# Kernel tuning notes

Hardware: AMD Instinct MI355X
Metric: run time of the kernel (lower is better)

## Reference

```python
import jax, jax.numpy as jnp
import numpy as np
from jax import lax

B, S, T = 32, 128, 128
E, H = 256, 512
VS, VT = 16000, 16000


def _gru_cell(h, x, Wih, Whh, bih, bhh):
    # PyTorch GRU gate order: r, z, n
    gi = x @ Wih.T + bih            # [B, 3H]
    gh = h @ Whh.T + bhh            # [B, 3H]
    ir, iz, inn = jnp.split(gi, 3, axis=-1)
    hr, hz, hn = jnp.split(gh, 3, axis=-1)
    r = jax.nn.sigmoid(ir + hr)
    z = jax.nn.sigmoid(iz + hz)
    n = jnp.tanh(inn + r * hn)
    return (1.0 - z) * n + z * h


def setup_inputs() -> dict:
    key = jax.random.key(0)
    ks = jax.random.split(key, 16)
    s = 0.05
    emb_src = (jax.random.normal(ks[2], (VS, E)) * s).at[0].set(0.0)  # padding_idx=0
    emb_tgt = (jax.random.normal(ks[3], (VT, E)) * s).at[0].set(0.0)
    return {
        "src": jax.random.randint(ks[0], (B, S), 0, VS),
        "tgt": jax.random.randint(ks[1], (B, T), 0, VT),
        "emb_src": emb_src,
        "emb_tgt": emb_tgt,
        "enc_Wih": jax.random.normal(ks[4], (3 * H, E)) * s,
        "enc_Whh": jax.random.normal(ks[5], (3 * H, H)) * s,
        "enc_bih": jnp.zeros((3 * H,), jnp.float32),
        "enc_bhh": jnp.zeros((3 * H,), jnp.float32),
        "dec_Wih": jax.random.normal(ks[6], (3 * H, E + H)) * s,
        "dec_Whh": jax.random.normal(ks[7], (3 * H, H)) * s,
        "dec_bih": jnp.zeros((3 * H,), jnp.float32),
        "dec_bhh": jnp.zeros((3 * H,), jnp.float32),
        "attn_W": jax.random.normal(ks[8], (H, 2 * H)) * s,   # nn.Linear(2H, H)
        "attn_b": jnp.zeros((H,), jnp.float32),
        "attn_v": jax.random.normal(ks[9], (H,)) * s,          # nn.Linear(H, 1, bias=False)
        "fc_W": jax.random.normal(ks[10], (VT, H)) * s,
        "fc_b": jnp.zeros((VT,), jnp.float32),
    }


def reference(src, tgt, emb_src, emb_tgt,
              enc_Wih, enc_Whh, enc_bih, enc_bhh,
              dec_Wih, dec_Whh, dec_bih, dec_bhh,
              attn_W, attn_b, attn_v, fc_W, fc_b):
    xs = emb_src[src]              # [B, S, E]
    ys = emb_tgt[tgt]              # [B, T, E]
    bsz = src.shape[0]

    # ---- encoder: single-layer GRU over src ----
    h0 = jnp.zeros((bsz, H), xs.dtype)

    def enc_step(h, x_t):
        h2 = _gru_cell(h, x_t, enc_Wih, enc_Whh, enc_bih, enc_bhh)
        return h2, h2

    h_enc, enc_seq = lax.scan(enc_step, h0, xs.transpose(1, 0, 2))
    enc_out = enc_seq.transpose(1, 0, 2)  # [B, S, H]

    # split attn weight: cat((hidden, enc_out)) @ W.T = h @ Wh.T + enc @ We.T
    Wh, We = attn_W[:, :H], attn_W[:, H:]
    enc_proj = enc_out @ We.T + attn_b    # [B, S, H], precomputed once

    # ---- decoder: per-step attention + GRU cell ----
    def dec_step(h, y_t):
        energy = jnp.tanh((h @ Wh.T)[:, None, :] + enc_proj)   # [B, S, H]
        scores = energy @ attn_v                               # [B, S]
        w = jax.nn.softmax(scores, axis=1)
        ctx = jnp.einsum('bs,bsh->bh', w, enc_out)             # [B, H]
        x = jnp.concatenate([y_t, ctx], axis=-1)               # [B, E+H]
        h2 = _gru_cell(h, x, dec_Wih, dec_Whh, dec_bih, dec_bhh)
        return h2, h2

    _, dec_seq = lax.scan(dec_step, h_enc, ys.transpose(1, 0, 2))
    dec_out = dec_seq.transpose(1, 0, 2)  # [B, T, H]

    logits = dec_out @ fc_W.T + fc_b      # [B, T, VT]
    return logits
```

## Files before the change

### kernel.cpp

```cpp
#include <hip/hip_runtime.h>
#include <hip/hip_bf16.h>

using bf16 = __hip_bfloat16;
typedef short bf16x8_t __attribute__((ext_vector_type(8)));
typedef float f32x4_t __attribute__((ext_vector_type(4)));

#define Bsz 32
#define Ssz 128
#define Tsz 128
#define Esz 256
#define Hsz 512
#define VTsz 16000

__device__ inline float sigm(float x)      { return 1.f / (1.f + __expf(-x)); }
__device__ inline float tanh_fast(float x) { return 1.f - 2.f / (1.f + __expf(2.f * x)); }

__device__ inline unsigned pack2(float x, float y) {
  unsigned short lo = __builtin_bit_cast(unsigned short, __float2bfloat16(x));
  unsigned short hi = __builtin_bit_cast(unsigned short, __float2bfloat16(y));
  return (unsigned)lo | ((unsigned)hi << 16);
}

__device__ inline uint4 f32x8_to_bf16x8(const float* s) {
  float4 a = *(const float4*)s;
  float4 b = *(const float4*)(s + 4);
  uint4 r;
  r.x = pack2(a.x, a.y); r.y = pack2(a.z, a.w);
  r.z = pack2(b.x, b.y); r.w = pack2(b.z, b.w);
  return r;
}

__global__ __launch_bounds__(256) void embed_gather(
    const int* __restrict__ src, const int* __restrict__ tgt,
    const float* __restrict__ es, const float* __restrict__ et,
    bf16* __restrict__ xs_b, bf16* __restrict__ ys_b)
{
  int idx = blockIdx.x * 256 + threadIdx.x;
  int which = idx >> 17;
  int c = idx & 131071;
  int row = c >> 5;
  int cc = c & 31;
  if (which == 0) {
    int tok = src[row];
    *(uint4*)(xs_b + (size_t)row * Esz + cc * 8) =
        f32x8_to_bf16x8(es + (size_t)tok * Esz + cc * 8);
  } else {
    int tok = tgt[row];
    *(uint4*)(ys_b + (size_t)row * Esz + cc * 8) =
        f32x8_to_bf16x8(et + (size_t)tok * Esz + cc * 8);
  }
}

__global__ __launch_bounds__(256) void transpose_w(
    const float* __restrict__ enc_Whh, const float* __restrict__ dec_Whh,
    const float* __restrict__ attn_W,  const float* __restrict__ dec_Wih,
    bf16* __restrict__ encWhh_t, bf16* __restrict__ Wcat_t, bf16* __restrict__ Wihctx_t)
{
  int idx = blockIdx.x * 256 + threadIdx.x;
  const int N1 = 512 * 1536, N2 = 512 * 2048;
  if (idx < N1) {
    int k = idx / 1536, j = idx % 1536;
    encWhh_t[idx] = __float2bfloat16(enc_Whh[(size_t)j * 512 + k]);
  } else if (idx < N1 + N2) {
    int r = idx - N1;
    int k = r / 2048, j = r % 2048;
    float v = (j < 1536) ? dec_Whh[(size_t)j * 512 + k]
                         : attn_W[(size_t)(j - 1536) * 1024 + k];
    Wcat_t[r] = __float2bfloat16(v);
  } else {
    int r = idx - N1 - N2;
    int k = r / 1536, j = r % 1536;
    Wihctx_t[r] = __float2bfloat16(dec_Wih[(size_t)j * 768 + 256 + k]);
  }
}

__global__ __launch_bounds__(256) void pack_weights(
    const float* __restrict__ enc_Wih, const float* __restrict__ dec_Wih,
    const float* __restrict__ attn_W,  const float* __restrict__ fc_W,
    bf16* __restrict__ encWih_b, bf16* __restrict__ decWihY_b,
    bf16* __restrict__ attnWe_b, bf16* __restrict__ fcW_b)
{
  int idx = blockIdx.x * 256 + threadIdx.x;
  const int R1 = 1536 * 256, R2 = 1536 * 256, R3 = 512 * 512;
  if (idx < R1) {
    encWih_b[idx] = __float2bfloat16(enc_Wih[idx]);
  } else if (idx < R1 + R2) {
    int r = idx - R1;
    int row = r >> 8, col = r & 255;
    decWihY_b[r] = __float2bfloat16(dec_Wih[(size_t)row * 768 + col]);
  } else if (idx < R1 + R2 + R3) {
    int r = idx - R1 - R2;
    int row = r >> 9, col = r & 511;
    attnWe_b[r] = __float2bfloat16(attn_W[(size_t)row * 1024 + 512 + col]);
  } else {
    int r = idx - R1 - R2 - R3;
    fcW_b[r] = __float2bfloat16(fc_W[r]);
  }
}

__global__ __launch_bounds__(256) void gemm_bt(
    const bf16* __restrict__ A, int lda,
    const bf16* __restrict__ B, int ldb,
    float* __restrict__ C, int ldc,
    const float* __restrict__ bias, int K)
{
  __shared__ __align__(16) bf16 As[128 * 64];
  __shared__ __align__(16) bf16 Bs[128 * 64];
  const int tid = threadIdx.x;
  const int m0 = blockIdx.y * 128, n0 = blockIdx.x * 128;
  const int lane = tid & 63, wave = tid >> 6;
  const int wm = (wave >> 1) * 64, wn = (wave & 1) * 64;
  const int fr = lane & 15, quad = lane >> 4;

  f32x4_t acc[4][4];
  const f32x4_t zero = {0.f, 0.f, 0.f, 0.f};
#pragma unroll
  for (int i = 0; i < 4; ++i)
#pragma unroll
    for (int j = 0; j < 4; ++j) acc[i][j] = zero;

  for (int k0 = 0; k0 < K; k0 += 64) {
    __syncthreads();
#pragma unroll
    for (int j = 0; j < 4; ++j) {
      int c = j * 256 + tid;
      int row = c >> 3, cc = c & 7;
      *(uint4*)(As + row * 64 + cc * 8) =
          *(const uint4*)(A + (size_t)(m0 + row) * lda + k0 + cc * 8);
      *(uint4*)(Bs + row * 64 + cc * 8) =
          *(const uint4*)(B + (size_t)(n0 + row) * ldb + k0 + cc * 8);
    }
    __syncthreads();
#pragma unroll
    for (int kk = 0; kk < 64; kk += 32) {
      bf16x8_t af[4], bfr[4];
#pragma unroll
      for (int mt = 0; mt < 4; ++mt)
        af[mt] = *(const bf16x8_t*)(As + (wm + mt * 16 + fr) * 64 + kk + quad * 8);
#pragma unroll
      for (int nt = 0; nt < 4; ++nt)
        bfr[nt] = *(const bf16x8_t*)(Bs + (wn + nt * 16 + fr) * 64 + kk + quad * 8);
#pragma unroll
      for (int mt = 0; mt < 4; ++mt)
#pragma unroll
        for (int nt = 0; nt < 4; ++nt)
          acc[mt][nt] = __builtin_amdgcn_mfma_f32_16x16x32_bf16(
              af[mt], bfr[nt], acc[mt][nt], 0, 0, 0);
    }
  }

#pragma unroll
  for (int mt = 0; mt < 4; ++mt) {
#pragma unroll
    for (int nt = 0; nt < 4; ++nt) {
      int n = n0 + wn + nt * 16 + fr;
      float bv = bias[n];
#pragma unroll
      for (int r = 0; r < 4; ++r) {
        int m = m0 + wm + mt * 16 + quad * 4 + r;
        C[(size_t)m * ldc + n] = acc[mt][nt][r] + bv;
      }
    }
  }
}

__global__ __launch_bounds__(256) void enc_step(
    const float* __restrict__ enc_gi, const bf16* __restrict__ Wt,
    const float* __restrict__ bhh, float* __restrict__ enc_out,
    bf16* __restrict__ enc_out_b, int t)
{
  __shared__ float hs[Hsz];
  __shared__ float ps[4][3][64];
  const int b = blockIdx.x >> 3, it = blockIdx.x & 7;
  const int tid = threadIdx.x, il = tid & 63, kg = tid >> 6;

  if (t == 0) {
    for (int i = tid; i < Hsz; i += 256) hs[i] = 0.f;
  } else {
    const float* hsrc = enc_out + ((size_t)b * Ssz + (t - 1)) * Hsz;
    for (int i = tid; i < Hsz; i += 256) hs[i] = hsrc[i];
  }
  __syncthreads();

  const int i = it * 64 + il;
  float pr = 0.f, pz = 0.f, pn = 0.f;
  for (int k = kg * 128; k < kg * 128 + 128; ++k) {
    const float hv = hs[k];
    const bf16* w = Wt + (size_t)k * 1536;
    pr += hv * (float)w[i];
    pz += hv * (float)w[Hsz + i];
    pn += hv * (float)w[2 * Hsz + i];
  }
  ps[kg][0][il] = pr; ps[kg][1][il] = pz; ps[kg][2][il] = pn;
  __syncthreads();

  if (tid < 64) {
    float ghr = ps[0][0][il] + ps[1][0][il] + ps[2][0][il] + ps[3][0][il] + bhh[i];
    float ghz = ps[0][1][il] + ps[1][1][il] + ps[2][1][il] + ps[3][1][il] + bhh[Hsz + i];
    float ghn = ps[0][2][il] + ps[1][2][il] + ps[2][2][il] + ps[3][2][il] + bhh[2 * Hsz + i];
    const float* gi = enc_gi + ((size_t)b * Ssz + t) * 1536;
    const float r = sigm(gi[i] + ghr);
    const float z = sigm(gi[Hsz + i] + ghz);
    const float n = tanh_fast(gi[2 * Hsz + i] + r * ghn);
    const float h2 = (1.f - z) * n + z * hs[i];
    const size_t o = ((size_t)b * Ssz + t) * Hsz + i;
    enc_out[o] = h2;
    enc_out_b[o] = __float2bfloat16(h2);
  }
}

__global__ __launch_bounds__(256) void dec_k1(
    const float* __restrict__ enc_out, const float* __restrict__ dec_seq,
    const bf16* __restrict__ Wcat_t, const float* __restrict__ dbhh,
    float* __restrict__ gh_ws, float* __restrict__ hW_ws, int t)
{
  __shared__ float hs[Hsz];
  __shared__ float ps[4][64];
  const int b = blockIdx.x >> 5, jt = blockIdx.x & 31;
  const int tid = threadIdx.x, il = tid & 63, kg = tid >> 6;

  const float* hsrc = (t == 0) ? (enc_out + ((size_t)b * Ssz + (Ssz - 1)) * Hsz)
                               : (dec_seq + ((size_t)b * Tsz + (t - 1)) * Hsz);
  for (int i = tid; i < Hsz; i += 256) hs[i] = hsrc[i];
  __syncthreads();

  const int j = jt * 64 + il;
  float p = 0.f;
  for (int k = kg * 128; k < kg * 128 + 128; ++k)
    p += hs[k] * (float)Wcat_t[(size_t)k * 2048 + j];
  ps[kg][il] = p;
  __syncthreads();

  if (tid < 64) {
    float s = ps[0][il] + ps[1][il] + ps[2][il] + ps[3][il];
    if (j < 1536) gh_ws[b * 1536 + j] = s + dbhh[j];
    else          hW_ws[b * Hsz + (j - 1536)] = s;
  }
}

__global__ __launch_bounds__(512) void dec_k2(
    const float* __restrict__ hW_ws, const float* __restrict__ enc_proj,
    const float* __restrict__ enc_out, const float* __restrict__ attn_v,
    float* __restrict__ ctx_ws)
{
  __shared__ float hw[Hsz], vv[Hsz], sc[Ssz], red[2], red2[2];
  const int b = blockIdx.x, tid = threadIdx.x;
  for (int i = tid; i < Hsz; i += 512) { hw[i] = hW_ws[b * Hsz + i]; vv[i] = attn_v[i]; }
  __syncthreads();

  const int wv = tid >> 6, lane = tid & 63;
  for (int s = wv; s < Ssz; s += 8) {
    const float* ep = enc_proj + ((size_t)b * Ssz + s) * Hsz;
    float pp = 0.f;
#pragma unroll
    for (int q = 0; q < 8; ++q) {
      int i = q * 64 + lane;
      pp += tanh_fast(hw[i] + ep[i]) * vv[i];
    }
#pragma unroll
    for (int off = 32; off; off >>= 1) pp += __shfl_down(pp, off);
    if (lane == 0) sc[s] = pp;
  }
  __syncthreads();

  if (tid < 128) {
    float v = sc[tid];
#pragma unroll
    for (int off = 32; off; off >>= 1) v = fmaxf(v, __shfl_down(v, off));
    if (lane == 0) red[tid >> 6] = v;
  }
  __syncthreads();
  const float mx = fmaxf(red[0], red[1]);
  if (tid < 128) {
    float e = __expf(sc[tid] - mx);
    sc[tid] = e;
    float v = e;
#pragma unroll
    for (int off = 32; off; off >>= 1) v += __shfl_down(v, off);
    if (lane == 0) red2[tid >> 6] = v;
  }
  __syncthreads();
  const float inv = 1.f / (red2[0] + red2[1]);

  for (int i = tid; i < Hsz; i += 512) {
    float a = 0.f;
    for (int s = 0; s < Ssz; ++s) a += sc[s] * enc_out[((size_t)b * Ssz + s) * Hsz + i];
    ctx_ws[b * Hsz + i] = a * inv;
  }
}

__global__ __launch_bounds__(256) void dec_k3(
    const float* __restrict__ ctx_ws, const bf16* __restrict__ Wihctx_t,
    const float* __restrict__ dec_gi_y, const float* __restrict__ gh_ws,
    const float* __restrict__ enc_out, float* __restrict__ dec_seq,
    bf16* __restrict__ dec_out_b, int t)
{
  __shared__ float cs[Hsz];
  __shared__ float ps[4][3][64];
  const int b = blockIdx.x >> 3, it = blockIdx.x & 7;
  const int tid = threadIdx.x, il = tid & 63, kg = tid >> 6;

  for (int i = tid; i < Hsz; i += 256) cs[i] = ctx_ws[b * Hsz + i];
  __syncthreads();

  const int i = it * 64 + il;
  float pr = 0.f, pz = 0.f, pn = 0.f;
  for (int k = kg * 128; k < kg * 128 + 128; ++k) {
    const float c = cs[k];
    const bf16* w = Wihctx_t + (size_t)k * 1536;
    pr += c * (float)w[i];
    pz += c * (float)w[Hsz + i];
    pn += c * (float)w[2 * Hsz + i];
  }
  ps[kg][0][il] = pr; ps[kg][1][il] = pz; ps[kg][2][il] = pn;
  __syncthreads();

  if (tid < 64) {
    const float* giy = dec_gi_y + ((size_t)b * Tsz + t) * 1536;
    const float* gh  = gh_ws + b * 1536;
    float gir = giy[i]           + ps[0][0][il] + ps[1][0][il] + ps[2][0][il] + ps[3][0][il];
    float giz = giy[Hsz + i]     + ps[0][1][il] + ps[1][1][il] + ps[2][1][il] + ps[3][1][il];
    float gin = giy[2 * Hsz + i] + ps[0][2][il] + ps[1][2][il] + ps[2][2][il] + ps[3][2][il];
    float ghr = gh[i], ghz = gh[Hsz + i], ghn = gh[2 * Hsz + i];
    const float* hsrc = (t == 0) ? (enc_out + ((size_t)b * Ssz + (Ssz - 1)) * Hsz)
                                 : (dec_seq + ((size_t)b * Tsz + (t - 1)) * Hsz);
    float hp = hsrc[i];
    const float r = sigm(gir + ghr);
    const float z = sigm(giz + ghz);
    const float n = tanh_fast(gin + r * ghn);
    const float h2 = (1.f - z) * n + z * hp;
    const size_t o = ((size_t)b * Tsz + t) * Hsz + i;
    dec_seq[o] = h2;
    dec_out_b[o] = __float2bfloat16(h2);
  }
}

extern "C" void kernel_launch(void* const* d_in, const int* in_sizes, int n_in,
                              void* d_out, int out_size, void* d_ws, size_t ws_size,
                              hipStream_t stream) {
  const int*   src      = (const int*)d_in[0];
  const int*   tgt      = (const int*)d_in[1];
  const float* emb_src  = (const float*)d_in[2];
  const float* emb_tgt  = (const float*)d_in[3];
  const float* enc_Wih  = (const float*)d_in[4];
  const float* enc_Whh  = (const float*)d_in[5];
  const float* enc_bih  = (const float*)d_in[6];
  const float* enc_bhh  = (const float*)d_in[7];
  const float* dec_Wih  = (const float*)d_in[8];
  const float* dec_Whh  = (const float*)d_in[9];
  const float* dec_bih  = (const float*)d_in[10];
  const float* dec_bhh  = (const float*)d_in[11];
  const float* attn_W   = (const float*)d_in[12];
  const float* attn_b   = (const float*)d_in[13];
  const float* attn_v   = (const float*)d_in[14];
  const float* fc_W     = (const float*)d_in[15];
  const float* fc_b     = (const float*)d_in[16];
  float* out = (float*)d_out;

  char* p = (char*)d_ws;
  auto alloc = [&](size_t n) { char* r = p; p += (n + 255) & ~(size_t)255; return r; };
  float* enc_gi    = (float*)alloc(4096ull * 1536 * 4);
  float* dec_gi_y  = (float*)alloc(4096ull * 1536 * 4);
  float* enc_out   = (float*)alloc(4096ull * 512 * 4);
  float* enc_proj  = (float*)alloc(4096ull * 512 * 4);
  float* dec_seq   = (float*)alloc(4096ull * 512 * 4);
  bf16*  enc_out_b = (bf16*)alloc(4096ull * 512 * 2);
  bf16*  dec_out_b = (bf16*)alloc(4096ull * 512 * 2);
  bf16*  xs_b      = (bf16*)alloc(4096ull * 256 * 2);
  bf16*  ys_b      = (bf16*)alloc(4096ull * 256 * 2);
  bf16*  encWhh_t  = (bf16*)alloc(512ull * 1536 * 2);
  bf16*  Wcat_t    = (bf16*)alloc(512ull * 2048 * 2);
  bf16*  Wihctx_t  = (bf16*)alloc(512ull * 1536 * 2);
  bf16*  encWih_b  = (bf16*)alloc(1536ull * 256 * 2);
  bf16*  decWihY_b = (bf16*)alloc(1536ull * 256 * 2);
  bf16*  attnWe_b  = (bf16*)alloc(512ull * 512 * 2);
  bf16*  fcW_b     = (bf16*)alloc(16000ull * 512 * 2);
  float* gh_ws     = (float*)alloc(32ull * 1536 * 4);
  float* hW_ws     = (float*)alloc(32ull * 512 * 4);
  float* ctx_ws    = (float*)alloc(32ull * 512 * 4);

  embed_gather<<<1024, 256, 0, stream>>>(src, tgt, emb_src, emb_tgt, xs_b, ys_b);
  transpose_w<<<10240, 256, 0, stream>>>(enc_Whh, dec_Whh, attn_W, dec_Wih,
                                         encWhh_t, Wcat_t, Wihctx_t);
  pack_weights<<<36096, 256, 0, stream>>>(enc_Wih, dec_Wih, attn_W, fc_W,
                                          encWih_b, decWihY_b, attnWe_b, fcW_b);

  gemm_bt<<<dim3(12, 32), 256, 0, stream>>>(xs_b, 256, encWih_b, 256,
                                            enc_gi, 1536, enc_bih, 256);
  gemm_bt<<<dim3(12, 32), 256, 0, stream>>>(ys_b, 256, decWihY_b, 256,
                                            dec_gi_y, 1536, dec_bih, 256);

  for (int t = 0; t < Ssz; ++t)
    enc_step<<<256, 256, 0, stream>>>(enc_gi, encWhh_t, enc_bhh, enc_out, enc_out_b, t);

  gemm_bt<<<dim3(4, 32), 256, 0, stream>>>(enc_out_b, 512, attnWe_b, 512,
                                           enc_proj, 512, attn_b, 512);

  for (int t = 0; t < Tsz; ++t) {
    dec_k1<<<1024, 256, 0, stream>>>(enc_out, dec_seq, Wcat_t, dec_bhh, gh_ws, hW_ws, t);
    dec_k2<<<32, 512, 0, stream>>>(hW_ws, enc_proj, enc_out, attn_v, ctx_ws);
    dec_k3<<<256, 256, 0, stream>>>(ctx_ws, Wihctx_t, dec_gi_y, gh_ws, enc_out,
                                    dec_seq, dec_out_b, t);
  }

  gemm_bt<<<dim3(125, 32), 256, 0, stream>>>(dec_out_b, 512, fcW_b, 512,
                                             out, VTsz, fc_b, 512);
}
```

Baseline: 5.728 ms.

## Replace per-timestep kernel launches with persistent cooperative kernels using grid sync

Folds the 128 encoder-step launches and the 384 decoder-step launches into two persistent cooperative kernels of 256 blocks each, with grid.sync() between dependent phases. This removes per-launch overhead and the inter-kernel gaps in the recurrent loops. The decoder's first phase now uses 256 blocks, each thread doing a full 512-length dot product instead of a 4-way split-K over 1024 blocks, so that phase has less parallelism. The attention phase runs on only 32 blocks while the rest wait at the grid barrier.

```diff
diff --git a/kernel.cpp b/kernel.cpp
--- a/kernel.cpp
+++ b/kernel.cpp
@@ -1,5 +1,8 @@
 #include <hip/hip_runtime.h>
 #include <hip/hip_bf16.h>
+#include <hip/hip_cooperative_groups.h>
+
+namespace cg = cooperative_groups;
 
 using bf16 = __hip_bfloat16;
 typedef short bf16x8_t __attribute__((ext_vector_type(8)));
@@ -164,174 +167,175 @@
   }
 }
 
-__global__ __launch_bounds__(256) void enc_step(
+__global__ __launch_bounds__(256) void enc_loop(
     const float* __restrict__ enc_gi, const bf16* __restrict__ Wt,
     const float* __restrict__ bhh, float* __restrict__ enc_out,
-    bf16* __restrict__ enc_out_b, int t)
-{
+    bf16* __restrict__ enc_out_b)
+{
+  cg::grid_group grid = cg::this_grid();
   __shared__ float hs[Hsz];
   __shared__ float ps[4][3][64];
   const int b = blockIdx.x >> 3, it = blockIdx.x & 7;
   const int tid = threadIdx.x, il = tid & 63, kg = tid >> 6;
-
-  if (t == 0) {
-    for (int i = tid; i < Hsz; i += 256) hs[i] = 0.f;
-  } else {
-    const float* hsrc = enc_out + ((size_t)b * Ssz + (t - 1)) * Hsz;
-    for (int i = tid; i < Hsz; i += 256) hs[i] = hsrc[i];
-  }
+  const int i = it * 64 + il;
+
+  for (int k = tid; k < Hsz; k += 256) hs[k] = 0.f;
   __syncthreads();
 
-  const int i = it * 64 + il;
-  float pr = 0.f, pz = 0.f, pn = 0.f;
-  for (int k = kg * 128; k < kg * 128 + 128; ++k) {
-    const float hv = hs[k];
-    const bf16* w = Wt + (size_t)k * 1536;
-    pr += hv * (float)w[i];
-    pz += hv * (float)w[Hsz + i];
-    pn += hv * (float)w[2 * Hsz + i];
-  }
-  ps[kg][0][il] = pr; ps[kg][1][il] = pz; ps[kg][2][il] = pn;
-  __syncthreads();
-
-  if (tid < 64) {
-    float ghr = ps[0][0][il] + ps[1][0][il] + ps[2][0][il] + ps[3][0][il] + bhh[i];
-    float ghz = ps[0][1][il] + ps[1][1][il] + ps[2][1][il] + ps[3][1][il] + bhh[Hsz + i];
-    float ghn = ps[0][2][il] + ps[1][2][il] + ps[2][2][il] + ps[3][2][il] + bhh[2 * Hsz + i];
-    const float* gi = enc_gi + ((size_t)b * Ssz + t) * 1536;
-    const float r = sigm(gi[i] + ghr);
-    const float z = sigm(gi[Hsz + i] + ghz);
-    const float n = tanh_fast(gi[2 * Hsz + i] + r * ghn);
-    const float h2 = (1.f - z) * n + z * hs[i];
-    const size_t o = ((size_t)b * Ssz + t) * Hsz + i;
-    enc_out[o] = h2;
-    enc_out_b[o] = __float2bfloat16(h2);
-  }
-}
-
-__global__ __launch_bounds__(256) void dec_k1(
-    const float* __restrict__ enc_out, const float* __restrict__ dec_seq,
-    const bf16* __restrict__ Wcat_t, const float* __restrict__ dbhh,
-    float* __restrict__ gh_ws, float* __restrict__ hW_ws, int t)
-{
+  for (int t = 0; t < Ssz; ++t) {
+    float pr = 0.f, pz = 0.f, pn = 0.f;
+    for (int k = kg * 128; k < kg * 128 + 128; ++k) {
+      const float hv = hs[k];
+      const bf16* w = Wt + (size_t)k * 1536;
+      pr += hv * (float)w[i];
+      pz += hv * (float)w[Hsz + i];
+      pn += hv * (float)w[2 * Hsz + i];
+    }
+    ps[kg][0][il] = pr; ps[kg][1][il] = pz; ps[kg][2][il] = pn;
+    __syncthreads();
+
+    if (tid < 64) {
+      float ghr = ps[0][0][il] + ps[1][0][il] + ps[2][0][il] + ps[3][0][il] + bhh[i];
+      float ghz = ps[0][1][il] + ps[1][1][il] + ps[2][1][il] + ps[3][1][il] + bhh[Hsz + i];
+      float ghn = ps[0][2][il] + ps[1][2][il] + ps[2][2][il] + ps[3][2][il] + bhh[2 * Hsz + i];
+      const float* gi = enc_gi + ((size_t)b * Ssz + t) * 1536;
+      const float r = sigm(gi[i] + ghr);
+      const float z = sigm(gi[Hsz + i] + ghz);
+      const float n = tanh_fast(gi[2 * Hsz + i] + r * ghn);
+      const float h2 = (1.f - z) * n + z * hs[i];
+      const size_t o = ((size_t)b * Ssz + t) * Hsz + i;
+      enc_out[o] = h2;
+      enc_out_b[o] = __float2bfloat16(h2);
+    }
+    grid.sync();
+
+    if (t + 1 < Ssz) {
+      const float* hsrc = enc_out + ((size_t)b * Ssz + t) * Hsz;
+      for (int k = tid; k < Hsz; k += 256) hs[k] = hsrc[k];
+      __syncthreads();
+    }
+  }
+}
+
+__global__ __launch_bounds__(256) void dec_loop(
+    const float* __restrict__ enc_out, const float* __restrict__ enc_proj,
+    const bf16* __restrict__ Wcat_t, const bf16* __restrict__ Wihctx_t,
+    const float* __restrict__ dec_gi_y, const float* __restrict__ dbhh,
+    const float* __restrict__ attn_v, float* __restrict__ dec_seq,
+    bf16* __restrict__ dec_out_b, float* __restrict__ gh_ws,
+    float* __restrict__ hW_ws, float* __restrict__ ctx_ws)
+{
+  cg::grid_group grid = cg::this_grid();
+  const int bid = blockIdx.x, tid = threadIdx.x;
+
+  const int b1 = bid >> 3, jt = bid & 7, j = jt * 256 + tid;
+  const int il = tid & 63, kg = tid >> 6;
+  const int i3 = (bid & 7) * 64 + il;
+
   __shared__ float hs[Hsz];
-  __shared__ float ps[4][64];
-  const int b = blockIdx.x >> 5, jt = blockIdx.x & 31;
-  const int tid = threadIdx.x, il = tid & 63, kg = tid >> 6;
-
-  const float* hsrc = (t == 0) ? (enc_out + ((size_t)b * Ssz + (Ssz - 1)) * Hsz)
-                               : (dec_seq + ((size_t)b * Tsz + (t - 1)) * Hsz);
-  for (int i = tid; i < Hsz; i += 256) hs[i] = hsrc[i];
-  __syncthreads();
-
-  const int j = jt * 64 + il;
-  float p = 0.f;
-  for (int k = kg * 128; k < kg * 128 + 128; ++k)
-    p += hs[k] * (float)Wcat_t[(size_t)k * 2048 + j];
-  ps[kg][il] = p;
-  __syncthreads();
-
-  if (tid < 64) {
-    float s = ps[0][il] + ps[1][il] + ps[2][il] + ps[3][il];
-    if (j < 1536) gh_ws[b * 1536 + j] = s + dbhh[j];
-    else          hW_ws[b * Hsz + (j - 1536)] = s;
-  }
-}
-
-__global__ __launch_bounds__(512) void dec_k2(
-    const float* __restrict__ hW_ws, const float* __restrict__ enc_proj,
-    const float* __restrict__ enc_out, const float* __restrict__ attn_v,
-    float* __restrict__ ctx_ws)
-{
-  __shared__ float hw[Hsz], vv[Hsz], sc[Ssz], red[2], red2[2];
-  const int b = blockIdx.x, tid = threadIdx.x;
-  for (int i = tid; i < Hsz; i += 512) { hw[i] = hW_ws[b * Hsz + i]; vv[i] = attn_v[i]; }
-  __syncthreads();
-
-  const int wv = tid >> 6, lane = tid & 63;
-  for (int s = wv; s < Ssz; s += 8) {
-    const float* ep = enc_proj + ((size_t)b * Ssz + s) * Hsz;
-    float pp = 0.f;
-#pragma unroll
-    for (int q = 0; q < 8; ++q) {
-      int i = q * 64 + lane;
-      pp += tanh_fast(hw[i] + ep[i]) * vv[i];
-    }
-#pragma unroll
-    for (int off = 32; off; off >>= 1) pp += __shfl_down(pp, off);
-    if (lane == 0) sc[s] = pp;
-  }
-  __syncthreads();
-
-  if (tid < 128) {
-    float v = sc[tid];
-#pragma unroll
-    for (int off = 32; off; off >>= 1) v = fmaxf(v, __shfl_down(v, off));
-    if (lane == 0) red[tid >> 6] = v;
-  }
-  __syncthreads();
-  const float mx = fmaxf(red[0], red[1]);
-  if (tid < 128) {
-    float e = __expf(sc[tid] - mx);
-    sc[tid] = e;
-    float v = e;
-#pragma unroll
-    for (int off = 32; off; off >>= 1) v += __shfl_down(v, off);
-    if (lane == 0) red2[tid >> 6] = v;
-  }
-  __syncthreads();
-  const float inv = 1.f / (red2[0] + red2[1]);
-
-  for (int i = tid; i < Hsz; i += 512) {
-    float a = 0.f;
-    for (int s = 0; s < Ssz; ++s) a += sc[s] * enc_out[((size_t)b * Ssz + s) * Hsz + i];
-    ctx_ws[b * Hsz + i] = a * inv;
-  }
-}
-
-__global__ __launch_bounds__(256) void dec_k3(
-    const float* __restrict__ ctx_ws, const bf16* __restrict__ Wihctx_t,
-    const float* __restrict__ dec_gi_y, const float* __restrict__ gh_ws,
-    const float* __restrict__ enc_out, float* __restrict__ dec_seq,
-    bf16* __restrict__ dec_out_b, int t)
-{
+  __shared__ float hw[Hsz], vv[Hsz], sc[Ssz];
+  __shared__ float red[2], red2[2];
   __shared__ float cs[Hsz];
   __shared__ float ps[4][3][64];
-  const int b = blockIdx.x >> 3, it = blockIdx.x & 7;
-  const int tid = threadIdx.x, il = tid & 63, kg = tid >> 6;
-
-  for (int i = tid; i < Hsz; i += 256) cs[i] = ctx_ws[b * Hsz + i];
-  __syncthreads();
-
-  const int i = it * 64 + il;
-  float pr = 0.f, pz = 0.f, pn = 0.f;
-  for (int k = kg * 128; k < kg * 128 + 128; ++k) {
-    const float c = cs[k];
-    const bf16* w = Wihctx_t + (size_t)k * 1536;
-    pr += c * (float)w[i];
-    pz += c * (float)w[Hsz + i];
-    pn += c * (float)w[2 * Hsz + i];
-  }
-  ps[kg][0][il] = pr; ps[kg][1][il] = pz; ps[kg][2][il] = pn;
-  __syncthreads();
-
-  if (tid < 64) {
-    const float* giy = dec_gi_y + ((size_t)b * Tsz + t) * 1536;
-    const float* gh  = gh_ws + b * 1536;
-    float gir = giy[i]           + ps[0][0][il] + ps[1][0][il] + ps[2][0][il] + ps[3][0][il];
-    float giz = giy[Hsz + i]     + ps[0][1][il] + ps[1][1][il] + ps[2][1][il] + ps[3][1][il];
-    float gin = giy[2 * Hsz + i] + ps[0][2][il] + ps[1][2][il] + ps[2][2][il] + ps[3][2][il];
-    float ghr = gh[i], ghz = gh[Hsz + i], ghn = gh[2 * Hsz + i];
-    const float* hsrc = (t == 0) ? (enc_out + ((size_t)b * Ssz + (Ssz - 1)) * Hsz)
-                                 : (dec_seq + ((size_t)b * Tsz + (t - 1)) * Hsz);
-    float hp = hsrc[i];
-    const float r = sigm(gir + ghr);
-    const float z = sigm(giz + ghz);
-    const float n = tanh_fast(gin + r * ghn);
-    const float h2 = (1.f - z) * n + z * hp;
-    const size_t o = ((size_t)b * Tsz + t) * Hsz + i;
-    dec_seq[o] = h2;
-    dec_out_b[o] = __float2bfloat16(h2);
+
+  if (bid < 32)
+    for (int k = tid; k < Hsz; k += 256) vv[k] = attn_v[k];
+
+  for (int t = 0; t < Tsz; ++t) {
+    {
+      const float* hsrc = (t == 0)
+          ? (enc_out + ((size_t)b1 * Ssz + (Ssz - 1)) * Hsz)
+          : (dec_seq + ((size_t)b1 * Tsz + (t - 1)) * Hsz);
+      for (int k = tid; k < Hsz; k += 256) hs[k] = hsrc[k];
+      __syncthreads();
+      float p = 0.f;
+#pragma unroll 8
+      for (int k = 0; k < Hsz; ++k)
+        p += hs[k] * (float)Wcat_t[(size_t)k * 2048 + j];
+      if (j < 1536) gh_ws[b1 * 1536 + j] = p + dbhh[j];
+      else          hW_ws[b1 * Hsz + (j - 1536)] = p;
+    }
+    grid.sync();
+
+    if (bid < 32) {
+      const int b = bid;
+      for (int k = tid; k < Hsz; k += 256) hw[k] = hW_ws[b * Hsz + k];
+      __syncthreads();
+      const int wv = tid >> 6, lane = tid & 63;
+      for (int s = wv; s < Ssz; s += 4) {
+        const float* ep = enc_proj + ((size_t)b * Ssz + s) * Hsz;
+        float pp = 0.f;
+#pragma unroll
+        for (int q = 0; q < 8; ++q) {
+          int k = q * 64 + lane;
+          pp += tanh_fast(hw[k] + ep[k]) * vv[k];
+        }
+#pragma unroll
+        for (int off = 32; off; off >>= 1) pp += __shfl_down(pp, off);
+        if (lane == 0) sc[s] = pp;
+      }
+      __syncthreads();
+      if (tid < 128) {
+        float v = sc[tid];
+#pragma unroll
+        for (int off = 32; off; off >>= 1) v = fmaxf(v, __shfl_down(v, off));
+        if (lane == 0) red[tid >> 6] = v;
+      }
+      __syncthreads();
+      const float mx = fmaxf(red[0], red[1]);
+      if (tid < 128) {
+        float e = __expf(sc[tid] - mx);
+        sc[tid] = e;
+        float v = e;
+#pragma unroll
+        for (int off = 32; off; off >>= 1) v += __shfl_down(v, off);
+        if (lane == 0) red2[tid >> 6] = v;
+      }
+      __syncthreads();
+      const float inv = 1.f / (red2[0] + red2[1]);
+      for (int k = tid; k < Hsz; k += 256) {
+        float a = 0.f;
+        for (int s = 0; s < Ssz; ++s)
+          a += sc[s] * enc_out[((size_t)b * Ssz + s) * Hsz + k];
+        ctx_ws[b * Hsz + k] = a * inv;
+      }
+    }
+    grid.sync();
+
+    {
+      for (int k = tid; k < Hsz; k += 256) cs[k] = ctx_ws[b1 * Hsz + k];
+      __syncthreads();
+      float pr = 0.f, pz = 0.f, pn = 0.f;
+      for (int k = kg * 128; k < kg * 128 + 128; ++k) {
+        const float c = cs[k];
+        const bf16* w = Wihctx_t + (size_t)k * 1536;
+        pr += c * (float)w[i3];
+        pz += c * (float)w[Hsz + i3];
+        pn += c * (float)w[2 * Hsz + i3];
+      }
+      ps[kg][0][il] = pr; ps[kg][1][il] = pz; ps[kg][2][il] = pn;
+      __syncthreads();
+      if (tid < 64) {
+        const float* giy = dec_gi_y + ((size_t)b1 * Tsz + t) * 1536;
+        const float* gh  = gh_ws + b1 * 1536;
+        float gir = giy[i3]           + ps[0][0][il] + ps[1][0][il] + ps[2][0][il] + ps[3][0][il];
+        float giz = giy[Hsz + i3]     + ps[0][1][il] + ps[1][1][il] + ps[2][1][il] + ps[3][1][il];
+        float gin = giy[2 * Hsz + i3] + ps[0][2][il] + ps[1][2][il] + ps[2][2][il] + ps[3][2][il];
+        float ghr = gh[i3], ghz = gh[Hsz + i3], ghn = gh[2 * Hsz + i3];
+        const float* hsrc = (t == 0)
+            ? (enc_out + ((size_t)b1 * Ssz + (Ssz - 1)) * Hsz)
+            : (dec_seq + ((size_t)b1 * Tsz + (t - 1)) * Hsz);
+        float hp = hsrc[i3];
+        const float r = sigm(gir + ghr);
+        const float z = sigm(giz + ghz);
+        const float n = tanh_fast(gin + r * ghn);
+        const float h2 = (1.f - z) * n + z * hp;
+        const size_t o = ((size_t)b1 * Tsz + t) * Hsz + i3;
+        dec_seq[o] = h2;
+        dec_out_b[o] = __float2bfloat16(h2);
+      }
+    }
+    grid.sync();
   }
 }
 
@@ -390,17 +394,23 @@
   gemm_bt<<<dim3(12, 32), 256, 0, stream>>>(ys_b, 256, decWihY_b, 256,
                                             dec_gi_y, 1536, dec_bih, 256);
 
-  for (int t = 0; t < Ssz; ++t)
-    enc_step<<<256, 256, 0, stream>>>(enc_gi, encWhh_t, enc_bhh, enc_out, enc_out_b, t);
+  {
+    void* args[] = {(void*)&enc_gi, (void*)&encWhh_t, (void*)&enc_bhh,
+                    (void*)&enc_out, (void*)&enc_out_b};
+    hipLaunchCooperativeKernel((void*)enc_loop, dim3(256), dim3(256),
+                               args, 0, stream);
+  }
 
   gemm_bt<<<dim3(4, 32), 256, 0, stream>>>(enc_out_b, 512, attnWe_b, 512,
                                            enc_proj, 512, attn_b, 512);
 
-  for (int t = 0; t < Tsz; ++t) {
-    dec_k1<<<1024, 256, 0, stream>>>(enc_out, dec_seq, Wcat_t, dec_bhh, gh_ws, hW_ws, t);
-    dec_k2<<<32, 512, 0, stream>>>(hW_ws, enc_proj, enc_out, attn_v, ctx_ws);
-    dec_k3<<<256, 256, 0, stream>>>(ctx_ws, Wihctx_t, dec_gi_y, gh_ws, enc_out,
-                                    dec_seq, dec_out_b, t);
+  {
+    void* args[] = {(void*)&enc_out, (void*)&enc_proj, (void*)&Wcat_t,
+                    (void*)&Wihctx_t, (void*)&dec_gi_y, (void*)&dec_bhh,
+                    (void*)&attn_v, (void*)&dec_seq, (void*)&dec_out_b,
+                    (void*)&gh_ws, (void*)&hW_ws, (void*)&ctx_ws};
+    hipLaunchCooperativeKernel((void*)dec_loop, dim3(256), dim3(256),
+                               args, 0, stream);
   }
 
   gemm_bt<<<dim3(125, 32), 256, 0, stream>>>(dec_out_b, 512, fcW_b, 512,
```

After: 21.53 ms. +275.9%, slower.
